# Optimization experiments

Measured on AMD Instinct MI355X. Metric: run time of the kernel, lower is better.

The kernel has to match this reference:

```python
import jax, jax.numpy as jnp
import numpy as np

N = 100000
E = 3200000
NFEAT, NHID, NCLASS = 256, 128, 40


def setup_inputs() -> dict:
    key = jax.random.key(0)
    ks = jax.random.split(key, 8)
    return {
        "x": jax.random.normal(ks[0], (N, NFEAT), dtype=jnp.float32),
        "edge_src": jax.random.randint(ks[1], (E,), 0, N, dtype=jnp.int32),
        "edge_dst": jax.random.randint(ks[2], (E,), 0, N, dtype=jnp.int32),
        "edge_w": jax.random.uniform(ks[3], (E,), dtype=jnp.float32),
        "W0": jax.random.normal(ks[4], (NFEAT, NHID), dtype=jnp.float32) * (2.0 / (NFEAT + NHID)) ** 0.5,
        "b0": jax.random.normal(ks[5], (1, NHID), dtype=jnp.float32) * 0.1,
        "W1": jax.random.normal(ks[6], (NHID, NCLASS), dtype=jnp.float32) * (2.0 / (NHID + NCLASS)) ** 0.5,
        "b1": jax.random.normal(ks[7], (1, NCLASS), dtype=jnp.float32) * 0.1,
    }


def _l2_normalize(h, eps=1e-12):
    # F.normalize(x, p=2, dim=1)
    nrm = jnp.sqrt(jnp.sum(h * h, axis=1, keepdims=True))
    return h / jnp.maximum(nrm, eps)


def reference(x, edge_src, edge_dst, edge_w, W0, b0, W1, b1):
    n_nodes = x.shape[0]

    def spmm(h):  # adj @ h with edge-list sparse adjacency
        return jax.ops.segment_sum(edge_w[:, None] * h[edge_src], edge_dst, num_segments=n_nodes)

    # layer 1: GraphConvolution = spmm(x @ W) + bias (dropout is identity in eval)
    h = spmm(x @ W0) + b0
    h = _l2_normalize(h)        # atg.Z1
    h = jax.nn.relu(h)          # atg.H1
    # layer 2
    z = spmm(h @ W1) + b1       # atg.Z2
    return jax.nn.log_softmax(z, axis=1)
```

## Files before the change

### kernel.cpp

```cpp
#include <hip/hip_runtime.h>
#include <math.h>

#define NN 100000
#define NE 3200000
#define NF 256
#define NH 128
#define NC 40

#define CH 8192
#define NBLK 391
#define NBUCK 782
#define HTOT (NBUCK * NBLK)
#define HS1 ((HTOT + 511) / 512)
#define NTILE 1563
#define NCP 32

typedef unsigned int uint;
typedef short short8 __attribute__((ext_vector_type(8)));
typedef float floatx4 __attribute__((ext_vector_type(4)));

__device__ __forceinline__ float bflo(uint v) { return __uint_as_float(v << 16); }
__device__ __forceinline__ float bfhi(uint v) { return __uint_as_float(v & 0xffff0000u); }
__device__ __forceinline__ unsigned short f2bf(float f) {
    const uint u = __float_as_uint(f);
    return (unsigned short)((u + 0x7fffu + ((u >> 16) & 1u)) >> 16);
}
__device__ __forceinline__ uint pack2bf(float a, float b) {
    return (uint)f2bf(a) | ((uint)f2bf(b) << 16);
}

union ABfrag { uint u[4]; short8 s; };

__device__ __forceinline__ void prep_body(int pidx,
                                          const float* __restrict__ W0,
                                          const float* __restrict__ W1,
                                          uint4* __restrict__ W0p,
                                          uint4* __restrict__ W1p) {
    const int idx = pidx * 256 + threadIdx.x;
    if (idx < 4096) {
        const int lane  = idx & 63;
        const int ntile = (idx >> 6) & 7;
        const int kstep = idx >> 9;
        const int n  = ntile * 16 + (lane & 15);
        const int kb = kstep * 32 + (lane >> 4) * 8;
        uint w[4];
#pragma unroll
        for (int ww = 0; ww < 4; ++ww)
            w[ww] = pack2bf(W0[(size_t)(kb + 2 * ww) * NH + n],
                            W0[(size_t)(kb + 2 * ww + 1) * NH + n]);
        W0p[idx] = make_uint4(w[0], w[1], w[2], w[3]);
    } else if (idx < 4096 + 768) {
        const int i2 = idx - 4096;
        const int lane  = i2 & 63;
        const int ntile = (i2 >> 6) % 3;
        const int kstep = (i2 >> 6) / 3;
        const int n  = ntile * 16 + (lane & 15);
        const int kb = kstep * 32 + (lane >> 4) * 8;
        uint w[4];
#pragma unroll
        for (int ww = 0; ww < 4; ++ww) {
            const float lo = (n < NC) ? W1[(size_t)(kb + 2 * ww) * NC + n] : 0.0f;
            const float hi = (n < NC) ? W1[(size_t)(kb + 2 * ww + 1) * NC + n] : 0.0f;
            w[ww] = pack2bf(lo, hi);
        }
        W1p[i2] = make_uint4(w[0], w[1], w[2], w[3]);
    }
}

__global__ __launch_bounds__(256) void k1_hist_prep(const int* __restrict__ edst,
                                                    int* __restrict__ hmat,
                                                    const float* __restrict__ W0,
                                                    const float* __restrict__ W1,
                                                    uint4* __restrict__ W0p,
                                                    uint4* __restrict__ W1p) {
    __shared__ uint h[NBUCK];
    const int bid = blockIdx.x;
    if (bid < 38 && (bid & 1)) { prep_body(bid >> 1, W0, W1, W0p, W1p); return; }
    const int b = (bid < 38) ? (bid >> 1) : (bid - 19);

    for (int i = threadIdx.x; i < NBUCK; i += 256) h[i] = 0;
    __syncthreads();
    const int e0 = b * CH, e1 = min(NE, e0 + CH);
    for (int e = e0 + threadIdx.x * 4; e + 3 < e1; e += 1024) {
        const int4 d4 = *(const int4*)(edst + e);
        atomicAdd(&h[((uint)d4.x) >> 7], 1u);
        atomicAdd(&h[((uint)d4.y) >> 7], 1u);
        atomicAdd(&h[((uint)d4.z) >> 7], 1u);
        atomicAdd(&h[((uint)d4.w) >> 7], 1u);
    }
    __syncthreads();
    for (int i = threadIdx.x; i < NBUCK; i += 256)
        hmat[(size_t)i * NBLK + b] = (int)h[i];
}

__global__ __launch_bounds__(512) void hscan1_k(int* __restrict__ hmat,
                                                int* __restrict__ partials) {
    __shared__ int s[512];
    const int t = threadIdx.x;
    const int i = blockIdx.x * 512 + t;
    const int v = (i < HTOT) ? hmat[i] : 0;
    s[t] = v;
    __syncthreads();
#pragma unroll
    for (int off = 1; off < 512; off <<= 1) {
        int a = (t >= off) ? s[t - off] : 0;
        __syncthreads();
        s[t] += a;
        __syncthreads();
    }
    if (i < HTOT) hmat[i] = s[t] - v;
    if (t == 511) partials[blockIdx.x] = s[t];
}

__global__ __launch_bounds__(1024) void hscan2_k(int* __restrict__ partials, int nb) {
    __shared__ int s[1024];
    const int t = threadIdx.x;
    const int v = (t < nb) ? partials[t] : 0;
    s[t] = v;
    __syncthreads();
#pragma unroll
    for (int off = 1; off < 1024; off <<= 1) {
        int a = (t >= off) ? s[t - off] : 0;
        __syncthreads();
        s[t] += a;
        __syncthreads();
    }
    if (t < nb) partials[t] = s[t] - v;
}

__global__ __launch_bounds__(256) void p1scat_k(const int* __restrict__ esrc,
                                                const int* __restrict__ edst,
                                                const float* __restrict__ ew,
                                                const int* __restrict__ hmat,
                                                const int* __restrict__ partials,
                                                uint2* __restrict__ ep1) {
    __shared__ uint base[NBUCK];
    const int b = blockIdx.x;
    for (int i = threadIdx.x; i < NBUCK; i += 256) {
        const int g = i * NBLK + b;
        base[i] = (uint)(hmat[g] + partials[g >> 9]);
    }
    __syncthreads();
    const int e0 = b * CH, e1 = min(NE, e0 + CH);
    for (int e = e0 + threadIdx.x; e < e1; e += 256) {
        const uint d = (uint)edst[e];
        const uint pos = atomicAdd(&base[d >> 7], 1u);
        ep1[pos] = make_uint2((uint)esrc[e] | ((d & 127u) << 17), __float_as_uint(ew[e]));
    }
}

__device__ __forceinline__ void p2_body(int bk,
                                        const int* __restrict__ hmat,
                                        const int* __restrict__ partials,
                                        const uint2* __restrict__ ep1,
                                        uint2* __restrict__ ep,
                                        int* __restrict__ rp) {
    const int gb = bk * NBLK;
    const int beg = hmat[gb] + partials[gb >> 9];
    int end;
    if (bk == NBUCK - 1) end = NE;
    else { const int ge = gb + NBLK; end = hmat[ge] + partials[ge >> 9]; }
    __shared__ uint cnt[128];
    __shared__ uint st[128];
    if (threadIdx.x < 128) cnt[threadIdx.x] = 0;
    __syncthreads();
    for (int j = beg + threadIdx.x; j < end; j += 256)
        atomicAdd(&cnt[(ep1[j].x >> 17) & 127u], 1u);
    __syncthreads();
    if (threadIdx.x < 128) st[threadIdx.x] = cnt[threadIdx.x];
    __syncthreads();
#pragma unroll
    for (int off = 1; off < 128; off <<= 1) {
        uint a = 0;
        if (threadIdx.x < 128 && threadIdx.x >= off) a = st[threadIdx.x - off];
        __syncthreads();
        if (threadIdx.x < 128) st[threadIdx.x] += a;
        __syncthreads();
    }
    if (threadIdx.x < 128) {
        const uint start = st[threadIdx.x] - cnt[threadIdx.x];
        const int d = bk * 128 + threadIdx.x;
        if (d < NN) rp[d] = beg + (int)start;
        cnt[threadIdx.x] = (uint)beg + start;
    }
    if (bk == 0 && threadIdx.x == 200) rp[NN] = NE;
    __syncthreads();
    for (int j = beg + threadIdx.x; j < end; j += 256) {
        const uint2 r = ep1[j];
        const uint pos = atomicAdd(&cnt[(r.x >> 17) & 127u], 1u);
        ep[pos] = r;
    }
}

__device__ __forceinline__ void gemm1_body(int bstart,
                                           const float* __restrict__ x,
                                           const uint4* __restrict__ W0p,
                                           unsigned short* __restrict__ xwh) {
    const int wave = threadIdx.x >> 6;
    const int lane = threadIdx.x & 63;
    const int quad = lane >> 4;
    const int mcol = lane & 15;

    for (int tile = bstart; tile < NTILE; tile += 512) {
        const int row  = tile * 64 + wave * 16 + mcol;
        const int rowc = min(row, NN - 1);
        const float* xr = x + (size_t)rowc * NF + quad * 8;

        floatx4 acc[8] = {};
        float4 lo = *(const float4*)(xr);
        float4 hi = *(const float4*)(xr + 4);
#pragma unroll
        for (int ks = 0; ks < 8; ++ks) {
            ABfrag a;
            a.u[0] = pack2bf(lo.x, lo.y);
            a.u[1] = pack2bf(lo.z, lo.w);
            a.u[2] = pack2bf(hi.x, hi.y);
            a.u[3] = pack2bf(hi.z, hi.w);
            if (ks < 7) {
                lo = *(const float4*)(xr + (ks + 1) * 32);
                hi = *(const float4*)(xr + (ks + 1) * 32 + 4);
            }
#pragma unroll
            for (int nt = 0; nt < 8; ++nt) {
                ABfrag b;
                const uint4 bw = W0p[(ks * 8 + nt) * 64 + lane];
                b.u[0] = bw.x; b.u[1] = bw.y; b.u[2] = bw.z; b.u[3] = bw.w;
                acc[nt] = __builtin_amdgcn_mfma_f32_16x16x32_bf16(a.s, b.s, acc[nt], 0, 0, 0);
            }
        }
        const int rowbase = tile * 64 + wave * 16 + quad * 4;
#pragma unroll
        for (int nt = 0; nt < 8; ++nt) {
#pragma unroll
            for (int r = 0; r < 4; ++r) {
                const int rr = rowbase + r;
                if (rr < NN) xwh[(size_t)rr * NH + nt * 16 + mcol] = f2bf(acc[nt][r]);
            }
        }
    }
}

__global__ __launch_bounds__(256) void k2_p2_gemm1(const int* __restrict__ hmat,
                                                   const int* __restrict__ partials,
                                                   const uint2* __restrict__ ep1,
                                                   uint2* __restrict__ ep,
                                                   int* __restrict__ rp,
                                                   const float* __restrict__ x,
                                                   const uint4* __restrict__ W0p,
                                                   unsigned short* __restrict__ xwh) {
    const int bid = blockIdx.x;
    if (bid < 1024 && (bid & 1)) { gemm1_body(bid >> 1, x, W0p, xwh); return; }
    const int bk = (bid < 1024) ? (bid >> 1) : (bid - 512);
    p2_body(bk, hmat, partials, ep1, ep, rp);
}

#define LD8(m, base) _Pragma("unroll") for (int u = 0; u < 8; ++u) m[u] = ep[(base) + u];
#define DEC8(s, w, m) _Pragma("unroll") for (int u = 0; u < 8; ++u) { \
        s[u] = ((uint)__builtin_amdgcn_readfirstlane(m[u].x)) & 0x1FFFFu; \
        w[u] = __uint_as_float((uint)__builtin_amdgcn_readfirstlane(m[u].y)); }
#define GAT8(v, s) _Pragma("unroll") for (int u = 0; u < 8; ++u) v[u] = xwb[(size_t)s[u] * 64 + t];
#define ACC8(v, w) _Pragma("unroll") for (int u = 0; u < 8; ++u) { \
        a0 = fmaf(w[u], bflo(v[u]), a0); a1 = fmaf(w[u], bfhi(v[u]), a1); }

__global__ __launch_bounds__(256) void spmm1n_g(const int* __restrict__ rp,
                                                const uint2* __restrict__ ep,
                                                const uint* __restrict__ xwb,
                                                const float* __restrict__ b0,
                                                uint* __restrict__ h2b) {
    const int n = blockIdx.x * 4 + (threadIdx.x >> 6);
    const int t = threadIdx.x & 63;
    const int beg = __builtin_amdgcn_readfirstlane(rp[n]);
    const int end = __builtin_amdgcn_readfirstlane(rp[n + 1]);
    float a0 = 0.f, a1 = 0.f;
    int j = beg;
    const int endf = beg + ((end - beg) & ~7);
    if (j < endf) {
        uint sA[8]; float wA[8]; uint vA[8];
        { uint2 m[8]; LD8(m, j); DEC8(sA, wA, m); GAT8(vA, sA); }
        int jn = j + 8;
        if (jn < endf) {
            uint sB[8]; float wB[8]; uint vB[8];
            { uint2 m[8]; LD8(m, jn); DEC8(sB, wB, m); GAT8(vB, sB); }
            jn += 8;
            for (;;) {
                if (jn < endf) {
                    uint2 m[8]; LD8(m, jn);
                    ACC8(vA, wA);
                    DEC8(sA, wA, m); GAT8(vA, sA);
                    jn += 8;
                } else { ACC8(vA, wA); ACC8(vB, wB); break; }
                if (jn < endf) {
                    uint2 m[8]; LD8(m, jn);
                    ACC8(vB, wB);
                    DEC8(sB, wB, m); GAT8(vB, sB);
                    jn += 8;
                } else { ACC8(vB, wB); ACC8(vA, wA); break; }
            }
        } else {
            ACC8(vA, wA);
        }
        j = endf;
    }
    for (; j < end; ++j) {
        const uint2 e = ep[j];
        const uint sx = ((uint)__builtin_amdgcn_readfirstlane(e.x)) & 0x1FFFFu;
        const float w = __uint_as_float((uint)__builtin_amdgcn_readfirstlane(e.y));
        const uint v = xwb[(size_t)sx * 64 + t];
        a0 = fmaf(w, bflo(v), a0); a1 = fmaf(w, bfhi(v), a1);
    }
    const float2 bb = *(const float2*)(b0 + 2 * t);
    const float v0 = a0 + bb.x, v1 = a1 + bb.y;
    float s = v0 * v0 + v1 * v1;
#pragma unroll
    for (int o = 1; o < 64; o <<= 1) s += __shfl_xor(s, o, 64);
    const float scale = 1.0f / fmaxf(sqrtf(s), 1e-12f);
    h2b[(size_t)n * 64 + t] = pack2bf(fmaxf(v0 * scale, 0.0f), fmaxf(v1 * scale, 0.0f));
}

__global__ __launch_bounds__(256) void gemm2_mfma(const uint* __restrict__ h2b,
                                                  const uint4* __restrict__ W1p,
                                                  unsigned short* __restrict__ hwh) {
    __shared__ __align__(16) uint4 sB[768];
    for (int i = threadIdx.x; i < 768; i += 256) sB[i] = W1p[i];
    __syncthreads();

    const int wave = threadIdx.x >> 6;
    const int lane = threadIdx.x & 63;
    const int quad = lane >> 4;
    const int mcol = lane & 15;
    const int row  = blockIdx.x * 64 + wave * 16 + mcol;
    const int rowc = min(row, NN - 1);
    const uint* hr = h2b + (size_t)rowc * 64;

    floatx4 acc[3] = {};
#pragma unroll
    for (int ks = 0; ks < 4; ++ks) {
        ABfrag a;
        const uint4 hv = *(const uint4*)(hr + ks * 16 + quad * 4);
        a.u[0] = hv.x; a.u[1] = hv.y; a.u[2] = hv.z; a.u[3] = hv.w;
#pragma unroll
        for (int nt = 0; nt < 3; ++nt) {
            ABfrag b;
            const uint4 bw = sB[(ks * 3 + nt) * 64 + lane];
            b.u[0] = bw.x; b.u[1] = bw.y; b.u[2] = bw.z; b.u[3] = bw.w;
            acc[nt] = __builtin_amdgcn_mfma_f32_16x16x32_bf16(a.s, b.s, acc[nt], 0, 0, 0);
        }
    }
    const int rowbase = blockIdx.x * 64 + wave * 16 + quad * 4;
#pragma unroll
    for (int nt = 0; nt < 3; ++nt) {
        const int f = nt * 16 + mcol;
#pragma unroll
        for (int r = 0; r < 4; ++r) {
            const int rr = rowbase + r;
            if (rr < NN)
                hwh[(size_t)rr * (2 * NCP) + f] = (f < NC) ? f2bf(acc[nt][r]) : (unsigned short)0;
        }
    }
#pragma unroll
    for (int r = 0; r < 4; ++r) {
        const int rr = rowbase + r;
        if (rr < NN) hwh[(size_t)rr * (2 * NCP) + 48 + mcol] = (unsigned short)0;
    }
}

#define DEC8L(s, w, m) _Pragma("unroll") for (int u = 0; u < 8; ++u) { \
        s[u] = m[u].x & 0x1FFFFu; w[u] = __uint_as_float(m[u].y); }
#define GAT8L(v, s) _Pragma("unroll") for (int u = 0; u < 8; ++u) v[u] = hwb[(size_t)s[u] * NCP + g];

__global__ __launch_bounds__(256) void spmm2l_g(const int* __restrict__ rp,
                                                const uint2* __restrict__ ep,
                                                const uint* __restrict__ hwb,
                                                const float* __restrict__ b1,
                                                float2* __restrict__ out2) {
    const int n = blockIdx.x * 8 + (threadIdx.x >> 5);
    const int g = threadIdx.x & 31;
    const int beg = rp[n], end = rp[n + 1];
    float a0 = 0.f, a1 = 0.f;
    int j = beg;
    const int endf = beg + ((end - beg) & ~7);
    if (j < endf) {
        uint sA[8]; float wA[8]; uint vA[8];
        { uint2 m[8]; LD8(m, j); DEC8L(sA, wA, m); GAT8L(vA, sA); }
        int jn = j + 8;
        if (jn < endf) {
            uint sB[8]; float wB[8]; uint vB[8];
            { uint2 m[8]; LD8(m, jn); DEC8L(sB, wB, m); GAT8L(vB, sB); }
            jn += 8;
            for (;;) {
                if (jn < endf) {
                    uint2 m[8]; LD8(m, jn);
                    ACC8(vA, wA);
                    DEC8L(sA, wA, m); GAT8L(vA, sA);
                    jn += 8;
                } else { ACC8(vA, wA); ACC8(vB, wB); break; }
                if (jn < endf) {
                    uint2 m[8]; LD8(m, jn);
                    ACC8(vB, wB);
                    DEC8L(sB, wB, m); GAT8L(vB, sB);
                    jn += 8;
                } else { ACC8(vB, wB); ACC8(vA, wA); break; }
            }
        } else {
            ACC8(vA, wA);
        }
        j = endf;
    }
    for (; j < end; ++j) {
        const uint2 e = ep[j];
        const uint v = hwb[(size_t)(e.x & 0x1FFFFu) * NCP + g];
        const float w = __uint_as_float(e.y);
        a0 = fmaf(w, bflo(v), a0); a1 = fmaf(w, bfhi(v), a1);
    }
    float bb0 = 0.f, bb1 = 0.f;
    if (g < 20) { const float2 bb = *(const float2*)(b1 + 2 * g); bb0 = bb.x; bb1 = bb.y; }
    a0 += bb0; a1 += bb1;
    float m = (g < 20) ? fmaxf(a0, a1) : -INFINITY;
#pragma unroll
    for (int o = 1; o < 32; o <<= 1) m = fmaxf(m, __shfl_xor(m, o, 32));
    float s = (g < 20) ? (expf(a0 - m) + expf(a1 - m)) : 0.f;
#pragma unroll
    for (int o = 1; o < 32; o <<= 1) s += __shfl_xor(s, o, 32);
    const float lse = logf(s);
    if (g < 20) out2[(size_t)n * 20 + g] = make_float2(a0 - m - lse, a1 - m - lse);
}

extern "C" void kernel_launch(void* const* d_in, const int* in_sizes, int n_in,
                              void* d_out, int out_size, void* d_ws, size_t ws_size,
                              hipStream_t stream) {
    const float* x    = (const float*)d_in[0];
    const int*   esrc = (const int*)d_in[1];
    const int*   edst = (const int*)d_in[2];
    const float* ew   = (const float*)d_in[3];
    const float* W0   = (const float*)d_in[4];
    const float* b0   = (const float*)d_in[5];
    const float* W1   = (const float*)d_in[6];
    const float* b1   = (const float*)d_in[7];
    float* out = (float*)d_out;

    size_t o = 0;
    uint*  xwb  = (uint*)d_ws + o;  o += (size_t)NN * 64;
    uint*  h2b  = (uint*)d_ws + o;  o += (size_t)NN * 64;
    uint2* ep1  = (uint2*)h2b;
    uint*  hwb  = (uint*)d_ws + o;  o += (size_t)NN * NCP;
    uint2* ep   = (uint2*)((uint*)d_ws + o); o += (size_t)NE * 2;
    int*   hmat = (int*)d_ws + o;   o += HTOT;
    int*   rp   = (int*)d_ws + o;   o += NN + 2;
    int*   partials = (int*)d_ws + o; o += 1024;
    if (o & 3) o += 4 - (o & 3);
    uint4* W0p  = (uint4*)((uint*)d_ws + o); o += 16384;
    uint4* W1p  = (uint4*)((uint*)d_ws + o); o += 3072;

    k1_hist_prep<<<410, 256, 0, stream>>>(edst, hmat, W0, W1, W0p, W1p);

    hscan1_k<<<HS1, 512, 0, stream>>>(hmat, partials);
    hscan2_k<<<1, 1024, 0, stream>>>(partials, HS1);
    p1scat_k<<<NBLK, 256, 0, stream>>>(esrc, edst, ew, hmat, partials, ep1);

    k2_p2_gemm1<<<1294, 256, 0, stream>>>(hmat, partials, ep1, ep, rp,
                                          x, W0p, (unsigned short*)xwb);

    spmm1n_g<<<NN / 4, 256, 0, stream>>>(rp, ep, xwb, b0, h2b);
    gemm2_mfma<<<NTILE, 256, 0, stream>>>(h2b, W1p, (unsigned short*)hwb);
    spmm2l_g<<<NN / 8, 256, 0, stream>>>(rp, ep, hwb, b1, (float2*)out);
}
```

Measured before the change: 543.9 us.

## Unfuse gemm1 from CSR pass, stage W0 in LDS, vectorize edge scatter

Splits the fused p2/gemm1 kernel into separate launches, with gemm1 moved early after the histogram prep. gemm1 now stages the packed W0 weights in 64KB of shared memory instead of reading them from global memory per fragment. The edge scatter kernel loads four edges per thread using vector loads. Unfusing loses the concurrent overlap of the sort pass with the GEMM, and the large LDS allocation may limit occupancy.

```diff
diff --git a/kernel.cpp b/kernel.cpp
--- a/kernel.cpp
+++ b/kernel.cpp
@@ -142,66 +142,46 @@
     }
     __syncthreads();
     const int e0 = b * CH, e1 = min(NE, e0 + CH);
-    for (int e = e0 + threadIdx.x; e < e1; e += 256) {
-        const uint d = (uint)edst[e];
-        const uint pos = atomicAdd(&base[d >> 7], 1u);
-        ep1[pos] = make_uint2((uint)esrc[e] | ((d & 127u) << 17), __float_as_uint(ew[e]));
-    }
-}
-
-__device__ __forceinline__ void p2_body(int bk,
-                                        const int* __restrict__ hmat,
-                                        const int* __restrict__ partials,
-                                        const uint2* __restrict__ ep1,
-                                        uint2* __restrict__ ep,
-                                        int* __restrict__ rp) {
-    const int gb = bk * NBLK;
-    const int beg = hmat[gb] + partials[gb >> 9];
-    int end;
-    if (bk == NBUCK - 1) end = NE;
-    else { const int ge = gb + NBLK; end = hmat[ge] + partials[ge >> 9]; }
-    __shared__ uint cnt[128];
-    __shared__ uint st[128];
-    if (threadIdx.x < 128) cnt[threadIdx.x] = 0;
-    __syncthreads();
-    for (int j = beg + threadIdx.x; j < end; j += 256)
-        atomicAdd(&cnt[(ep1[j].x >> 17) & 127u], 1u);
-    __syncthreads();
-    if (threadIdx.x < 128) st[threadIdx.x] = cnt[threadIdx.x];
-    __syncthreads();
-#pragma unroll
-    for (int off = 1; off < 128; off <<= 1) {
-        uint a = 0;
-        if (threadIdx.x < 128 && threadIdx.x >= off) a = st[threadIdx.x - off];
-        __syncthreads();
-        if (threadIdx.x < 128) st[threadIdx.x] += a;
-        __syncthreads();
-    }
-    if (threadIdx.x < 128) {
-        const uint start = st[threadIdx.x] - cnt[threadIdx.x];
-        const int d = bk * 128 + threadIdx.x;
-        if (d < NN) rp[d] = beg + (int)start;
-        cnt[threadIdx.x] = (uint)beg + start;
-    }
-    if (bk == 0 && threadIdx.x == 200) rp[NN] = NE;
-    __syncthreads();
-    for (int j = beg + threadIdx.x; j < end; j += 256) {
-        const uint2 r = ep1[j];
-        const uint pos = atomicAdd(&cnt[(r.x >> 17) & 127u], 1u);
-        ep[pos] = r;
-    }
-}
-
-__device__ __forceinline__ void gemm1_body(int bstart,
-                                           const float* __restrict__ x,
-                                           const uint4* __restrict__ W0p,
-                                           unsigned short* __restrict__ xwh) {
+    for (int e = e0 + threadIdx.x * 4; e + 3 < e1; e += 1024) {
+        const int4   s4 = *(const int4*)(esrc + e);
+        const int4   d4 = *(const int4*)(edst + e);
+        const float4 w4 = *(const float4*)(ew + e);
+        {
+            const uint d = (uint)d4.x;
+            const uint pos = atomicAdd(&base[d >> 7], 1u);
+            ep1[pos] = make_uint2((uint)s4.x | ((d & 127u) << 17), __float_as_uint(w4.x));
+        }
+        {
+            const uint d = (uint)d4.y;
+            const uint pos = atomicAdd(&base[d >> 7], 1u);
+            ep1[pos] = make_uint2((uint)s4.y | ((d & 127u) << 17), __float_as_uint(w4.y));
+        }
+        {
+            const uint d = (uint)d4.z;
+            const uint pos = atomicAdd(&base[d >> 7], 1u);
+            ep1[pos] = make_uint2((uint)s4.z | ((d & 127u) << 17), __float_as_uint(w4.z));
+        }
+        {
+            const uint d = (uint)d4.w;
+            const uint pos = atomicAdd(&base[d >> 7], 1u);
+            ep1[pos] = make_uint2((uint)s4.w | ((d & 127u) << 17), __float_as_uint(w4.w));
+        }
+    }
+}
+
+__global__ __launch_bounds__(256) void gemm1_mfma(const float* __restrict__ x,
+                                                  const uint4* __restrict__ W0p,
+                                                  unsigned short* __restrict__ xwh) {
+    __shared__ __align__(16) uint4 sB[4096];
+    for (int i = threadIdx.x; i < 4096; i += 256) sB[i] = W0p[i];
+    __syncthreads();
+
     const int wave = threadIdx.x >> 6;
     const int lane = threadIdx.x & 63;
     const int quad = lane >> 4;
     const int mcol = lane & 15;
 
-    for (int tile = bstart; tile < NTILE; tile += 512) {
+    for (int tile = blockIdx.x; tile < NTILE; tile += 512) {
         const int row  = tile * 64 + wave * 16 + mcol;
         const int rowc = min(row, NN - 1);
         const float* xr = x + (size_t)rowc * NF + quad * 8;
@@ -223,7 +203,7 @@
 #pragma unroll
             for (int nt = 0; nt < 8; ++nt) {
                 ABfrag b;
-                const uint4 bw = W0p[(ks * 8 + nt) * 64 + lane];
+                const uint4 bw = sB[(ks * 8 + nt) * 64 + lane];
                 b.u[0] = bw.x; b.u[1] = bw.y; b.u[2] = bw.z; b.u[3] = bw.w;
                 acc[nt] = __builtin_amdgcn_mfma_f32_16x16x32_bf16(a.s, b.s, acc[nt], 0, 0, 0);
             }
@@ -240,18 +220,47 @@
     }
 }
 
-__global__ __launch_bounds__(256) void k2_p2_gemm1(const int* __restrict__ hmat,
-                                                   const int* __restrict__ partials,
-                                                   const uint2* __restrict__ ep1,
-                                                   uint2* __restrict__ ep,
-                                                   int* __restrict__ rp,
-                                                   const float* __restrict__ x,
-                                                   const uint4* __restrict__ W0p,
-                                                   unsigned short* __restrict__ xwh) {
-    const int bid = blockIdx.x;
-    if (bid < 1024 && (bid & 1)) { gemm1_body(bid >> 1, x, W0p, xwh); return; }
-    const int bk = (bid < 1024) ? (bid >> 1) : (bid - 512);
-    p2_body(bk, hmat, partials, ep1, ep, rp);
+__global__ __launch_bounds__(256) void p2_k(const int* __restrict__ hmat,
+                                            const int* __restrict__ partials,
+                                            const uint2* __restrict__ ep1,
+                                            uint2* __restrict__ ep,
+                                            int* __restrict__ rp) {
+    const int bk = blockIdx.x;
+    const int gb = bk * NBLK;
+    const int beg = hmat[gb] + partials[gb >> 9];
+    int end;
+    if (bk == NBUCK - 1) end = NE;
+    else { const int ge = gb + NBLK; end = hmat[ge] + partials[ge >> 9]; }
+    __shared__ uint cnt[128];
+    __shared__ uint st[128];
+    if (threadIdx.x < 128) cnt[threadIdx.x] = 0;
+    __syncthreads();
+    for (int j = beg + threadIdx.x; j < end; j += 256)
+        atomicAdd(&cnt[(ep1[j].x >> 17) & 127u], 1u);
+    __syncthreads();
+    if (threadIdx.x < 128) st[threadIdx.x] = cnt[threadIdx.x];
+    __syncthreads();
+#pragma unroll
+    for (int off = 1; off < 128; off <<= 1) {
+        uint a = 0;
+        if (threadIdx.x < 128 && threadIdx.x >= off) a = st[threadIdx.x - off];
+        __syncthreads();
+        if (threadIdx.x < 128) st[threadIdx.x] += a;
+        __syncthreads();
+    }
+    if (threadIdx.x < 128) {
+        const uint start = st[threadIdx.x] - cnt[threadIdx.x];
+        const int d = bk * 128 + threadIdx.x;
+        if (d < NN) rp[d] = beg + (int)start;
+        cnt[threadIdx.x] = (uint)beg + start;
+    }
+    if (bk == 0 && threadIdx.x == 200) rp[NN] = NE;
+    __syncthreads();
+    for (int j = beg + threadIdx.x; j < end; j += 256) {
+        const uint2 r = ep1[j];
+        const uint pos = atomicAdd(&cnt[(r.x >> 17) & 127u], 1u);
+        ep[pos] = r;
+    }
 }
 
 #define LD8(m, base) _Pragma("unroll") for (int u = 0; u < 8; ++u) m[u] = ep[(base) + u];
@@ -452,13 +461,12 @@
     uint4* W1p  = (uint4*)((uint*)d_ws + o); o += 3072;
 
     k1_hist_prep<<<410, 256, 0, stream>>>(edst, hmat, W0, W1, W0p, W1p);
+    gemm1_mfma<<<512, 256, 0, stream>>>(x, W0p, (unsigned short*)xwb);
 
     hscan1_k<<<HS1, 512, 0, stream>>>(hmat, partials);
     hscan2_k<<<1, 1024, 0, stream>>>(partials, HS1);
     p1scat_k<<<NBLK, 256, 0, stream>>>(esrc, edst, ew, hmat, partials, ep1);
-
-    k2_p2_gemm1<<<1294, 256, 0, stream>>>(hmat, partials, ep1, ep, rp,
-                                          x, W0p, (unsigned short*)xwb);
+    p2_k<<<NBUCK, 256, 0, stream>>>(hmat, partials, ep1, ep, rp);
 
     spmm1n_g<<<NN / 4, 256, 0, stream>>>(rp, ep, xwb, b0, h2b);
     gemm2_mfma<<<NTILE, 256, 0, stream>>>(h2b, W1p, (unsigned short*)hwb);
```

Result: faster. 510.5 us (-6.1%).
